# Kernel tuning notes

Hardware: AMD Instinct MI355X
Metric: run time of the kernel (lower is better)

The kernel has to match this reference:

```python
import jax, jax.numpy as jnp
import numpy as np

N, E, F_IN, H, L = 100000, 1600000, 256, 128, 4
ALPHA, THETA, EPS = 0.1, 0.5, 1e-5


def setup_inputs() -> dict:
    key = jax.random.key(0)
    ks = jax.random.split(key, 6)
    x = jax.random.normal(ks[0], (N, F_IN), dtype=jnp.float32)
    edge_index = jax.random.randint(ks[1], (2, E), 0, N, dtype=jnp.int32)
    lin0_w = jax.random.normal(ks[2], (F_IN, H), dtype=jnp.float32) / np.sqrt(F_IN)
    lin0_b = jnp.zeros((H,), dtype=jnp.float32)
    conv_w = jax.random.normal(ks[3], (L, H, H), dtype=jnp.float32) / np.sqrt(H)
    bn_gamma = jnp.ones((L - 1, H), dtype=jnp.float32)
    bn_beta = jnp.zeros((L - 1, H), dtype=jnp.float32)
    return {"x": x, "edge_index": edge_index, "lin0_w": lin0_w, "lin0_b": lin0_b,
            "conv_w": conv_w, "bn_gamma": bn_gamma, "bn_beta": bn_beta}


def reference(x, edge_index, lin0_w, lin0_b, conv_w, bn_gamma, bn_beta):
    n = x.shape[0]
    loops = jnp.arange(n, dtype=edge_index.dtype)
    row = jnp.concatenate([edge_index[0], loops])  # source
    col = jnp.concatenate([edge_index[1], loops])  # target
    # GCN symmetric normalization with self-loops: D^{-1/2}(A+I)D^{-1/2}
    deg = jax.ops.segment_sum(jnp.ones_like(col, dtype=x.dtype), col, num_segments=n)
    dinv = jnp.where(deg > 0, jax.lax.rsqrt(deg), 0.0)
    norm = (dinv[row] * dinv[col])[:, None]  # [E+N, 1]

    def prop(h):  # sparse aggregation: out[c] += norm * h[r]
        return jax.ops.segment_sum(h[row] * norm, col, num_segments=n)

    # GCNConv input layer
    z = prop(x @ lin0_w) + lin0_b
    x0 = z
    for i in range(L):
        h = prop(z)
        beta = float(np.log(THETA / (i + 1) + 1.0))
        s = (1.0 - ALPHA) * h + ALPHA * x0          # identity mapping to initial features
        z = (1.0 - beta) * s + beta * (s @ conv_w[i])  # shared_weights GCN2Conv
        if i < L - 1:
            mu = jnp.mean(z, axis=0)
            var = jnp.mean((z - mu) ** 2, axis=0)
            z = (z - mu) * jax.lax.rsqrt(var + EPS) * bn_gamma[i] + bn_beta[i]
            z = jax.nn.relu(z)
    return z
```

## Files before the change

kernel.cpp:

```cpp
#include <hip/hip_runtime.h>
#include <hip/hip_bf16.h>
#include <math.h>

#define H 128
#define EPS_BN 1e-5f
#define RSTATS 16

typedef __attribute__((ext_vector_type(8))) short short8;
typedef __attribute__((ext_vector_type(4))) float f32x4;

__device__ __forceinline__ float bf2f(ushort u){
  union { float f; uint v; } x; x.v = ((uint)u) << 16; return x.f;
}
__device__ __forceinline__ ushort f2bf(float f){
  union { float f; uint v; } x; x.f = f;
  uint v = x.v;
  uint r = v + 0x7fff + ((v >> 16) & 1);
  return (ushort)(r >> 16);
}

__device__ __forceinline__ void acc8(float* a, uint4 v, float wt){
  a[0] += wt*bf2f((ushort)(v.x & 0xffff)); a[1] += wt*bf2f((ushort)(v.x >> 16));
  a[2] += wt*bf2f((ushort)(v.y & 0xffff)); a[3] += wt*bf2f((ushort)(v.y >> 16));
  a[4] += wt*bf2f((ushort)(v.z & 0xffff)); a[5] += wt*bf2f((ushort)(v.z >> 16));
  a[6] += wt*bf2f((ushort)(v.w & 0xffff)); a[7] += wt*bf2f((ushort)(v.w >> 16));
}


__global__ void k_count(const int* __restrict__ col, int E, int* __restrict__ cnt){
  int i = blockIdx.x*blockDim.x + threadIdx.x;
  if (i < E) atomicAdd(&cnt[col[i]], 1);
}

__global__ void k_scan1(const int* __restrict__ cnt, int* __restrict__ off,
                        int* __restrict__ bsum, float* __restrict__ dinv, int n){
  __shared__ int s[1024];
  int t = threadIdx.x;
  int i = blockIdx.x*1024 + t;
  int v = (i < n) ? cnt[i] : 0;
  if (i < n) dinv[i] = rsqrtf((float)v + 1.0f);
  s[t] = v; __syncthreads();
  for (int d = 1; d < 1024; d <<= 1){
    int x = (t >= d) ? s[t-d] : 0;
    __syncthreads();
    s[t] += x;
    __syncthreads();
  }
  if (i < n) off[i] = s[t] - v;
  if (t == 1023) bsum[blockIdx.x] = s[1023];
}

__global__ void k_scan2(int* bsum, int nb){
  int l = threadIdx.x;
  int carry = 0;
  for (int b0 = 0; b0 < nb; b0 += 64){
    int i = b0 + l;
    int orig = (i < nb) ? bsum[i] : 0;
    int v = orig;
    #pragma unroll
    for (int d = 1; d < 64; d <<= 1){
      int x = __shfl_up(v, d);
      if (l >= d) v += x;
    }
    if (i < nb) bsum[i] = carry + v - orig;
    carry += __shfl(v, 63);
  }
}

__global__ void k_scan3(int* __restrict__ off, int* __restrict__ cursor,
                        const int* __restrict__ bsum, int n, int Etot){
  int i = blockIdx.x*blockDim.x + threadIdx.x;
  if (i < n){ int o = off[i] + bsum[i >> 10]; off[i] = o; cursor[i] = o; }
  if (i == 0) off[n] = Etot;
}

__global__ void k_fill(const int* __restrict__ row, const int* __restrict__ col, int E,
                       const float* __restrict__ dinv, int* __restrict__ cursor,
                       uint2* __restrict__ edge){
  int i = blockIdx.x*blockDim.x + threadIdx.x;
  if (i < E){
    int c = col[i], r = row[i];
    int p = atomicAdd(&cursor[c], 1);
    edge[p] = make_uint2((uint)r, __float_as_uint(dinv[r]*dinv[c]));
  }
}


__global__ __launch_bounds__(1024) void k_dhist(
    const int* __restrict__ cnt, int* __restrict__ dh, int n){
  __shared__ int lh[256];
  int t = threadIdx.x;
  if (t < 256) lh[t] = 0;
  __syncthreads();
  int i = blockIdx.x*1024 + t;
  if (i < n){
    int d = cnt[i]; if (d > 255) d = 255;
    atomicAdd(&lh[d], 1);
  }
  __syncthreads();
  if (t < 256 && lh[t]) atomicAdd(&dh[t], lh[t]);
}

__global__ void k_dscan(int* __restrict__ dh){
  __shared__ int s[256];
  int t = threadIdx.x;
  int v = dh[t];
  s[t] = v; __syncthreads();
  for (int d = 1; d < 256; d <<= 1){
    int x = (t >= d) ? s[t-d] : 0;
    __syncthreads();
    s[t] += x;
    __syncthreads();
  }
  dh[t] = s[t] - v;
}

__global__ __launch_bounds__(1024) void k_dperm(
    const int* __restrict__ cnt, int* __restrict__ dh,
    int* __restrict__ perm, int n){
  __shared__ int lh[256];
  __shared__ int lbase[256];
  int t = threadIdx.x;
  if (t < 256) lh[t] = 0;
  __syncthreads();
  int i = blockIdx.x*1024 + t;
  int d = 0, li = 0;
  if (i < n){
    d = cnt[i]; if (d > 255) d = 255;
    li = atomicAdd(&lh[d], 1);
  }
  __syncthreads();
  if (t < 256){
    int c = lh[t];
    lbase[t] = c ? atomicAdd(&dh[t], c) : 0;
  }
  __syncthreads();
  if (i < n) perm[lbase[d] + li] = i;
}


__global__ void k_prepw(const float* __restrict__ lin0_w, const float* __restrict__ conv_w,
                        ushort* __restrict__ lin0T, ushort* __restrict__ WpT,
                        float b0, float b1, float b2, float b3){
  int i = blockIdx.x*blockDim.x + threadIdx.x;
  if (i < 128*256){
    int nn = i >> 8, k = i & 255;
    lin0T[i] = f2bf(lin0_w[k*128 + nn]);
  } else if (i < 128*256 + 4*128*128){
    int j = i - 128*256;
    int ll = j >> 14, rc = j & 16383;
    int nn = rc >> 7, k = rc & 127;
    float beta = (ll==0)?b0:(ll==1)?b1:(ll==2)?b2:b3;
    float v = beta * conv_w[ll*16384 + k*128 + nn];
    if (k == nn) v += 1.0f - beta;
    WpT[j] = f2bf(v);
  }
}


__device__ __forceinline__ void gather_edges(
    float* a, const ushort* __restrict__ zin, const uint2* __restrict__ edge,
    int e0, int e1, int lr){
  int e = e0;
  for (; e + 3 < e1; e += 4){
    uint2 er0 = edge[e],   er1 = edge[e+1];
    uint2 er2 = edge[e+2], er3 = edge[e+3];
    uint4 v0 = *(const uint4*)(zin + (size_t)er0.x*H + lr*8);
    uint4 v1 = *(const uint4*)(zin + (size_t)er1.x*H + lr*8);
    uint4 v2 = *(const uint4*)(zin + (size_t)er2.x*H + lr*8);
    uint4 v3 = *(const uint4*)(zin + (size_t)er3.x*H + lr*8);
    acc8(a, v0, __uint_as_float(er0.y));
    acc8(a, v1, __uint_as_float(er1.y));
    acc8(a, v2, __uint_as_float(er2.y));
    acc8(a, v3, __uint_as_float(er3.y));
  }
  for (; e < e1; ++e){
    uint2 er = edge[e];
    uint4 v = *(const uint4*)(zin + (size_t)er.x*H + lr*8);
    acc8(a, v, __uint_as_float(er.y));
  }
}


__global__ __launch_bounds__(256) void k_prop0(
    const ushort* __restrict__ h, const int* __restrict__ off,
    const uint2* __restrict__ edge, const float* __restrict__ dinv,
    const float* __restrict__ bias, const int* __restrict__ perm,
    ushort* __restrict__ x0, int n){
  int pq = (blockIdx.x*blockDim.x + threadIdx.x) >> 4;
  if (pq >= n) return;
  int gq = perm[n - 1 - pq];
  int lr = threadIdx.x & 15;
  float a[8];
  #pragma unroll
  for (int j = 0; j < 8; ++j) a[j] = 0.f;
  float wc = dinv[gq]; wc *= wc;
  uint4 vs = *(const uint4*)(h + (size_t)gq*H + lr*8);
  gather_edges(a, h, edge, off[gq], off[gq+1], lr);
  acc8(a, vs, wc);
  float4 b0 = *(const float4*)(bias + lr*8);
  float4 b1 = *(const float4*)(bias + lr*8 + 4);
  uint4 pk;
  pk.x = (uint)f2bf(a[0]+b0.x) | ((uint)f2bf(a[1]+b0.y) << 16);
  pk.y = (uint)f2bf(a[2]+b0.z) | ((uint)f2bf(a[3]+b0.w) << 16);
  pk.z = (uint)f2bf(a[4]+b1.x) | ((uint)f2bf(a[5]+b1.y) << 16);
  pk.w = (uint)f2bf(a[6]+b1.z) | ((uint)f2bf(a[7]+b1.w) << 16);
  *(uint4*)(x0 + (size_t)gq*H + lr*8) = pk;
}


template<bool STATS, bool OUTF32, bool SAMEX0>
__global__ __launch_bounds__(256) void k_layer(
    const ushort* __restrict__ zin, const ushort* __restrict__ x0,
    const int* __restrict__ off, const uint2* __restrict__ edge,
    const float* __restrict__ dinv, const ushort* __restrict__ BT,
    const int* __restrict__ perm,
    void* __restrict__ zout, float* __restrict__ stats, int n)
{
  __shared__ ushort Sm[32*128];
  __shared__ int pm[32];
  int t = threadIdx.x;
  int w = t >> 6, l = t & 63;
  int lr = l & 15, q = l >> 4;
  int base = blockIdx.x * 32;
  if (t < 32) pm[t] = (base + t < n) ? perm[n - 1 - (base + t)] : -1;
  __syncthreads();

  #pragma unroll
  for (int g2 = 0; g2 < 2; ++g2){
    int row  = w*8 + g2*4 + q;
    int node = pm[row];
    float a[8];
    #pragma unroll
    for (int j = 0; j < 8; ++j) a[j] = 0.f;
    uint4 pk = make_uint4(0u,0u,0u,0u);
    if (node >= 0){
      float wc = dinv[node]; wc *= wc;
      uint4 vs = *(const uint4*)(zin + (size_t)node*H + lr*8);
      gather_edges(a, zin, edge, off[node], off[node+1], lr);
      acc8(a, vs, wc);
      uint4 xv = SAMEX0 ? vs : *(const uint4*)(x0 + (size_t)node*H + lr*8);
      float s0 = 0.9f*a[0] + 0.1f*bf2f((ushort)(xv.x & 0xffff));
      float s1 = 0.9f*a[1] + 0.1f*bf2f((ushort)(xv.x >> 16));
      float s2 = 0.9f*a[2] + 0.1f*bf2f((ushort)(xv.y & 0xffff));
      float s3 = 0.9f*a[3] + 0.1f*bf2f((ushort)(xv.y >> 16));
      float s4 = 0.9f*a[4] + 0.1f*bf2f((ushort)(xv.z & 0xffff));
      float s5 = 0.9f*a[5] + 0.1f*bf2f((ushort)(xv.z >> 16));
      float s6 = 0.9f*a[6] + 0.1f*bf2f((ushort)(xv.w & 0xffff));
      float s7 = 0.9f*a[7] + 0.1f*bf2f((ushort)(xv.w >> 16));
      pk.x = (uint)f2bf(s0) | ((uint)f2bf(s1) << 16);
      pk.y = (uint)f2bf(s2) | ((uint)f2bf(s3) << 16);
      pk.z = (uint)f2bf(s4) | ((uint)f2bf(s5) << 16);
      pk.w = (uint)f2bf(s6) | ((uint)f2bf(s7) << 16);
    }
    *(uint4*)(&Sm[row*128 + ((lr ^ (row & 15))*8)]) = pk;
  }

  short8 bfr[2][4];
  #pragma unroll
  for (int c = 0; c < 2; ++c)
    #pragma unroll
    for (int ks = 0; ks < 4; ++ks)
      bfr[c][ks] = *(const short8*)(BT + (size_t)(w*32 + c*16 + lr)*H + ks*32 + q*8);

  __syncthreads();

  f32x4 acc[2][2];
  #pragma unroll
  for (int rt = 0; rt < 2; ++rt){
    acc[rt][0] = (f32x4){0.f,0.f,0.f,0.f};
    acc[rt][1] = (f32x4){0.f,0.f,0.f,0.f};
  }
  #pragma unroll
  for (int rt = 0; rt < 2; ++rt){
    int row = rt*16 + lr;
    #pragma unroll
    for (int ks = 0; ks < 4; ++ks){
      short8 af = *(const short8*)(&Sm[row*128 + (((ks*4 + q) ^ (row & 15))*8)]);
      acc[rt][0] = __builtin_amdgcn_mfma_f32_16x16x32_bf16(af, bfr[0][ks], acc[rt][0], 0,0,0);
      acc[rt][1] = __builtin_amdgcn_mfma_f32_16x16x32_bf16(af, bfr[1][ks], acc[rt][1], 0,0,0);
    }
  }

  #pragma unroll
  for (int rt = 0; rt < 2; ++rt){
    #pragma unroll
    for (int c = 0; c < 2; ++c){
      #pragma unroll
      for (int j2 = 0; j2 < 4; ++j2){
        int rowl = rt*16 + q*4 + j2;
        int nodeo = pm[rowl];
        float v = acc[rt][c][j2];
        if (OUTF32){
          if (nodeo >= 0)
            ((float*)zout)[(size_t)nodeo*H + w*32 + c*16 + lr] = v;
        } else {
          float other = __shfl(v, l ^ 1);
          if (!(lr & 1) && nodeo >= 0){
            uint pk = (uint)f2bf(v) | ((uint)f2bf(other) << 16);
            ((uint*)zout)[(size_t)nodeo*64 + w*16 + c*8 + (lr >> 1)] = pk;
          }
        }
      }
    }
  }
  if (STATS){
    #pragma unroll
    for (int c = 0; c < 2; ++c){
      float sv = 0.f, sq = 0.f;
      #pragma unroll
      for (int rt = 0; rt < 2; ++rt)
        #pragma unroll
        for (int j2 = 0; j2 < 4; ++j2){
          float v = acc[rt][c][j2];
          sv += v; sq += v*v;
        }
      sv += __shfl(sv, l ^ 16); sv += __shfl(sv, l ^ 32);
      sq += __shfl(sq, l ^ 16); sq += __shfl(sq, l ^ 32);
      if (q == 0){
        float* st = stats + (size_t)(blockIdx.x & (RSTATS-1))*256;
        atomicAdd(&st[w*32 + c*16 + lr], sv);
        atomicAdd(&st[128 + w*32 + c*16 + lr], sq);
      }
    }
  }
}


__global__ void k_bnfinal(float* __restrict__ stats, const float* __restrict__ gamma,
                          const float* __restrict__ beta, float* __restrict__ scsh,
                          float inv_n){
  int f = threadIdx.x;
  float s = 0.f, s2 = 0.f;
  for (int r = 0; r < RSTATS; ++r){
    s  += stats[r*256 + f];
    s2 += stats[r*256 + 128 + f];
    stats[r*256 + f] = 0.f;
    stats[r*256 + 128 + f] = 0.f;
  }
  float mu  = s * inv_n;
  float var = s2 * inv_n - mu*mu;
  float sc  = rsqrtf(var + EPS_BN) * gamma[f];
  scsh[f]       = sc;
  scsh[128 + f] = beta[f] - mu*sc;
}


__global__ __launch_bounds__(256) void k_bnapply(
    uint4* __restrict__ z, const float* __restrict__ scsh, int n16){
  int i = blockIdx.x*blockDim.x + threadIdx.x;
  if (i >= n16) return;
  int f8 = (i & 15) * 8;
  uint4 v = z[i];
  uint r[4];
  #pragma unroll
  for (int p = 0; p < 4; ++p){
    uint  u  = (&v.x)[p];
    float z0 = bf2f((ushort)(u & 0xffff));
    float z1 = bf2f((ushort)(u >> 16));
    float y0 = fmaxf(fmaf(z0, scsh[f8 + p*2],     scsh[128 + f8 + p*2]),     0.f);
    float y1 = fmaxf(fmaf(z1, scsh[f8 + p*2 + 1], scsh[128 + f8 + p*2 + 1]), 0.f);
    r[p] = (uint)f2bf(y0) | ((uint)f2bf(y1) << 16);
  }
  z[i] = make_uint4(r[0], r[1], r[2], r[3]);
}


__global__ __launch_bounds__(256) void k_gemm0(
    const float* __restrict__ Af, const ushort* __restrict__ BT,
    ushort* __restrict__ Cb, int n){
  const int K = 256;
  __shared__ ushort As[64*32];
  __shared__ ushort Bs[128*32];
  int t = threadIdx.x;
  int br = blockIdx.x * 64;
  int w = t >> 6, l = t & 63;
  int lr = l & 15, lk = l >> 4;
  int swz = (lr >> 1) & 3;

  f32x4 acc[8];
  #pragma unroll
  for (int i = 0; i < 8; ++i) acc[i] = (f32x4){0.f,0.f,0.f,0.f};

  int sar = t >> 2;
  int sab = t & 3;
  int sa_off = sar*32 + ((sab ^ ((sar>>1)&3))*8);

  for (int k0 = 0; k0 < K; k0 += 32){
    int grow = br + sar;
    float4 v0 = make_float4(0.f,0.f,0.f,0.f), v1 = v0;
    if (grow < n){
      v0 = *(const float4*)(Af + (size_t)grow*K + k0 + sab*8);
      v1 = *(const float4*)(Af + (size_t)grow*K + k0 + sab*8 + 4);
    }
    ushort tmp[8] = {f2bf(v0.x),f2bf(v0.y),f2bf(v0.z),f2bf(v0.w),
                     f2bf(v1.x),f2bf(v1.y),f2bf(v1.z),f2bf(v1.w)};
    *(uint4*)(&As[sa_off]) = *(const uint4*)tmp;
    #pragma unroll
    for (int i = 0; i < 2; ++i){
      int qq = t + i*256;
      int nrow = qq >> 2, bb = qq & 3;
      uint4 v = *(const uint4*)(BT + (size_t)nrow*K + k0 + bb*8);
      *(uint4*)(&Bs[nrow*32 + ((bb ^ ((nrow>>1)&3))*8)]) = v;
    }
    __syncthreads();
    short8 af = *(const short8*)(&As[(w*16+lr)*32 + ((lk ^ swz)*8)]);
    #pragma unroll
    for (int tn = 0; tn < 8; ++tn){
      short8 bfv = *(const short8*)(&Bs[(tn*16+lr)*32 + ((lk ^ swz)*8)]);
      acc[tn] = __builtin_amdgcn_mfma_f32_16x16x32_bf16(af, bfv, acc[tn], 0, 0, 0);
    }
    __syncthreads();
  }
  int orow = br + w*16 + lk*4;
  #pragma unroll
  for (int tn = 0; tn < 8; ++tn){
    #pragma unroll
    for (int j = 0; j < 4; ++j){
      float mine  = acc[tn][j];
      float other = __shfl(mine, l ^ 1);
      if (!(l & 1) && (orow + j) < n){
        uint pk = (uint)f2bf(mine) | ((uint)f2bf(other) << 16);
        ((uint*)Cb)[(size_t)(orow+j)*64 + tn*8 + (lr >> 1)] = pk;
      }
    }
  }
}


extern "C" void kernel_launch(void* const* d_in, const int* in_sizes, int n_in,
                              void* d_out, int out_size, void* d_ws, size_t ws_size,
                              hipStream_t stream){
  const float* x        = (const float*)d_in[0];
  const int*   ei       = (const int*)  d_in[1];
  const float* lin0_w   = (const float*)d_in[2];
  const float* lin0_b   = (const float*)d_in[3];
  const float* conv_w   = (const float*)d_in[4];
  const float* bn_gamma = (const float*)d_in[5];
  const float* bn_beta  = (const float*)d_in[6];
  float* out = (float*)d_out;

  int N = in_sizes[0] / 256;
  int E = in_sizes[1] / 2;
  const int* row = ei;
  const int* col = ei + E;

  char* ws = (char*)d_ws;
  size_t p = 0;
  auto alloc = [&](size_t bytes)->char*{
    char* r = ws + p; p = (p + bytes + 255) & ~(size_t)255; return r;
  };
  int*    cnt    = (int*)   alloc((size_t)N*4);
  int*    off    = (int*)   alloc((size_t)(N+1)*4);
  int*    cursor = (int*)   alloc((size_t)N*4);
  float*  dinv   = (float*) alloc((size_t)N*4);
  int*    bsum   = (int*)   alloc(512*4);
  int*    dh     = (int*)   alloc(256*4);
  int*    perm   = (int*)   alloc((size_t)N*4);
  uint2*  edge   = (uint2*) alloc((size_t)E*8);
  ushort* zb     = (ushort*)alloc((size_t)N*H*2);
  ushort* sb     = (ushort*)alloc((size_t)N*H*2);
  ushort* x0b    = (ushort*)alloc((size_t)N*H*2);
  ushort* lin0T  = (ushort*)alloc(128*256*2);
  ushort* WpT    = (ushort*)alloc(4*128*128*2);
  float*  stats  = (float*) alloc(RSTATS*256*4);
  float*  scsh   = (float*) alloc(2*128*4);

  float betas[4];
  for (int i = 0; i < 4; ++i) betas[i] = logf(0.5f/(float)(i+1) + 1.0f);
  float inv_n = 1.0f/(float)N;

  hipMemsetAsync(cnt, 0, (size_t)N*4, stream);
  hipMemsetAsync(dh, 0, 256*4, stream);
  k_count<<<(E+255)/256, 256, 0, stream>>>(col, E, cnt);
  int nb1k = (N + 1023)/1024;
  k_dhist<<<nb1k, 1024, 0, stream>>>(cnt, dh, N);
  k_dscan<<<1, 256, 0, stream>>>(dh);
  k_dperm<<<nb1k, 1024, 0, stream>>>(cnt, dh, perm, N);
  k_scan1<<<nb1k, 1024, 0, stream>>>(cnt, off, bsum, dinv, N);
  k_scan2<<<1, 64, 0, stream>>>(bsum, nb1k);
  k_scan3<<<(N+255)/256, 256, 0, stream>>>(off, cursor, bsum, N, E);
  k_fill <<<(E+255)/256, 256, 0, stream>>>(row, col, E, dinv, cursor, edge);

  k_prepw<<<(128*256 + 4*128*128 + 255)/256, 256, 0, stream>>>(
      lin0_w, conv_w, lin0T, WpT, betas[0], betas[1], betas[2], betas[3]);

  int gemm_blocks = (N + 63)/64;
  int lay_blocks  = (N + 31)/32;
  int prop_blocks = (N + 15)/16;
  int bn_blocks   = ((N*16) + 255)/256;

  k_gemm0<<<gemm_blocks, 256, 0, stream>>>(x, lin0T, sb, N);
  k_prop0<<<prop_blocks, 256, 0, stream>>>(sb, off, edge, dinv, lin0_b, perm, x0b, N);

  hipMemsetAsync(stats, 0, RSTATS*256*4, stream);

  k_layer<true,false,true><<<lay_blocks, 256, 0, stream>>>(
      x0b, x0b, off, edge, dinv, WpT + 0*128*128, perm, sb, stats, N);
  k_bnfinal<<<1, 128, 0, stream>>>(stats, bn_gamma + 0*H, bn_beta + 0*H, scsh, inv_n);
  k_bnapply<<<bn_blocks, 256, 0, stream>>>((uint4*)sb, scsh, N*16);

  k_layer<true,false,false><<<lay_blocks, 256, 0, stream>>>(
      sb, x0b, off, edge, dinv, WpT + 1*128*128, perm, zb, stats, N);
  k_bnfinal<<<1, 128, 0, stream>>>(stats, bn_gamma + 1*H, bn_beta + 1*H, scsh, inv_n);
  k_bnapply<<<bn_blocks, 256, 0, stream>>>((uint4*)zb, scsh, N*16);

  k_layer<true,false,false><<<lay_blocks, 256, 0, stream>>>(
      zb, x0b, off, edge, dinv, WpT + 2*128*128, perm, sb, stats, N);
  k_bnfinal<<<1, 128, 0, stream>>>(stats, bn_gamma + 2*H, bn_beta + 2*H, scsh, inv_n);
  k_bnapply<<<bn_blocks, 256, 0, stream>>>((uint4*)sb, scsh, N*16);

  k_layer<false,true,false><<<lay_blocks, 256, 0, stream>>>(
      sb, x0b, off, edge, dinv, WpT + 3*128*128, perm, out, nullptr, N);
}
```

Baseline: 612.6 us.

## Store node features in degree-sorted permuted order to make self and output accesses contiguous

Intermediate feature buffers are now indexed by position in the degree-sorted permutation instead of the original node id. An inverse permutation is built so edge sources are stored as permuted indices. The degree scan is reversed so the perm array itself is descending and needs no n-1-i flip. The first GEMM gathers input rows through perm. Self-feature loads, x0 loads and bf16 output stores become contiguous per block, which removes scattered row accesses. Gather locality over neighbours changes with the new ordering, and the extra iperm array plus the perm lookup in the GEMM add a little setup cost.

New measurement: 603.2 us. Within noise of the previous version (-1.5%).

```diff
diff --git a/kernel.cpp b/kernel.cpp
--- a/kernel.cpp
+++ b/kernel.cpp
@@ -75,13 +75,13 @@
 }
 
 __global__ void k_fill(const int* __restrict__ row, const int* __restrict__ col, int E,
-                       const float* __restrict__ dinv, int* __restrict__ cursor,
-                       uint2* __restrict__ edge){
+                       const float* __restrict__ dinv, const int* __restrict__ iperm,
+                       int* __restrict__ cursor, uint2* __restrict__ edge){
   int i = blockIdx.x*blockDim.x + threadIdx.x;
   if (i < E){
     int c = col[i], r = row[i];
     int p = atomicAdd(&cursor[c], 1);
-    edge[p] = make_uint2((uint)r, __float_as_uint(dinv[r]*dinv[c]));
+    edge[p] = make_uint2((uint)iperm[r], __float_as_uint(dinv[r]*dinv[c]));
   }
 }
 
@@ -104,7 +104,7 @@
 __global__ void k_dscan(int* __restrict__ dh){
   __shared__ int s[256];
   int t = threadIdx.x;
-  int v = dh[t];
+  int v = dh[255 - t];
   s[t] = v; __syncthreads();
   for (int d = 1; d < 256; d <<= 1){
     int x = (t >= d) ? s[t-d] : 0;
@@ -112,12 +112,12 @@
     s[t] += x;
     __syncthreads();
   }
-  dh[t] = s[t] - v;
+  dh[255 - t] = s[t] - v;
 }
 
 __global__ __launch_bounds__(1024) void k_dperm(
     const int* __restrict__ cnt, int* __restrict__ dh,
-    int* __restrict__ perm, int n){
+    int* __restrict__ perm, int* __restrict__ iperm, int n){
   __shared__ int lh[256];
   __shared__ int lbase[256];
   int t = threadIdx.x;
@@ -135,7 +135,11 @@
     lbase[t] = c ? atomicAdd(&dh[t], c) : 0;
   }
   __syncthreads();
-  if (i < n) perm[lbase[d] + li] = i;
+  if (i < n){
+    int pos = lbase[d] + li;
+    perm[pos] = i;
+    iperm[i] = pos;
+  }
 }
 
 
@@ -189,13 +193,13 @@
     ushort* __restrict__ x0, int n){
   int pq = (blockIdx.x*blockDim.x + threadIdx.x) >> 4;
   if (pq >= n) return;
-  int gq = perm[n - 1 - pq];
+  int gq = perm[pq];
   int lr = threadIdx.x & 15;
   float a[8];
   #pragma unroll
   for (int j = 0; j < 8; ++j) a[j] = 0.f;
   float wc = dinv[gq]; wc *= wc;
-  uint4 vs = *(const uint4*)(h + (size_t)gq*H + lr*8);
+  uint4 vs = *(const uint4*)(h + (size_t)pq*H + lr*8);
   gather_edges(a, h, edge, off[gq], off[gq+1], lr);
   acc8(a, vs, wc);
   float4 b0 = *(const float4*)(bias + lr*8);
@@ -205,7 +209,7 @@
   pk.y = (uint)f2bf(a[2]+b0.z) | ((uint)f2bf(a[3]+b0.w) << 16);
   pk.z = (uint)f2bf(a[4]+b1.x) | ((uint)f2bf(a[5]+b1.y) << 16);
   pk.w = (uint)f2bf(a[6]+b1.z) | ((uint)f2bf(a[7]+b1.w) << 16);
-  *(uint4*)(x0 + (size_t)gq*H + lr*8) = pk;
+  *(uint4*)(x0 + (size_t)pq*H + lr*8) = pk;
 }
 
 
@@ -223,23 +227,24 @@
   int w = t >> 6, l = t & 63;
   int lr = l & 15, q = l >> 4;
   int base = blockIdx.x * 32;
-  if (t < 32) pm[t] = (base + t < n) ? perm[n - 1 - (base + t)] : -1;
+  if (t < 32) pm[t] = (base + t < n) ? perm[base + t] : -1;
   __syncthreads();
 
   #pragma unroll
   for (int g2 = 0; g2 < 2; ++g2){
     int row  = w*8 + g2*4 + q;
     int node = pm[row];
+    int grow = base + row;
     float a[8];
     #pragma unroll
     for (int j = 0; j < 8; ++j) a[j] = 0.f;
     uint4 pk = make_uint4(0u,0u,0u,0u);
     if (node >= 0){
       float wc = dinv[node]; wc *= wc;
-      uint4 vs = *(const uint4*)(zin + (size_t)node*H + lr*8);
+      uint4 vs = *(const uint4*)(zin + (size_t)grow*H + lr*8);
       gather_edges(a, zin, edge, off[node], off[node+1], lr);
       acc8(a, vs, wc);
-      uint4 xv = SAMEX0 ? vs : *(const uint4*)(x0 + (size_t)node*H + lr*8);
+      uint4 xv = SAMEX0 ? vs : *(const uint4*)(x0 + (size_t)grow*H + lr*8);
       float s0 = 0.9f*a[0] + 0.1f*bf2f((ushort)(xv.x & 0xffff));
       float s1 = 0.9f*a[1] + 0.1f*bf2f((ushort)(xv.x >> 16));
       float s2 = 0.9f*a[2] + 0.1f*bf2f((ushort)(xv.y & 0xffff));
@@ -289,16 +294,17 @@
       #pragma unroll
       for (int j2 = 0; j2 < 4; ++j2){
         int rowl = rt*16 + q*4 + j2;
-        int nodeo = pm[rowl];
         float v = acc[rt][c][j2];
         if (OUTF32){
+          int nodeo = pm[rowl];
           if (nodeo >= 0)
             ((float*)zout)[(size_t)nodeo*H + w*32 + c*16 + lr] = v;
         } else {
+          int growl = base + rowl;
           float other = __shfl(v, l ^ 1);
-          if (!(lr & 1) && nodeo >= 0){
+          if (!(lr & 1) && growl < n){
             uint pk = (uint)f2bf(v) | ((uint)f2bf(other) << 16);
-            ((uint*)zout)[(size_t)nodeo*64 + w*16 + c*8 + (lr >> 1)] = pk;
+            ((uint*)zout)[(size_t)growl*64 + w*16 + c*8 + (lr >> 1)] = pk;
           }
         }
       }
@@ -368,15 +374,18 @@
 
 __global__ __launch_bounds__(256) void k_gemm0(
     const float* __restrict__ Af, const ushort* __restrict__ BT,
-    ushort* __restrict__ Cb, int n){
+    const int* __restrict__ perm, ushort* __restrict__ Cb, int n){
   const int K = 256;
   __shared__ ushort As[64*32];
   __shared__ ushort Bs[128*32];
+  __shared__ int pmr[64];
   int t = threadIdx.x;
   int br = blockIdx.x * 64;
   int w = t >> 6, l = t & 63;
   int lr = l & 15, lk = l >> 4;
   int swz = (lr >> 1) & 3;
+  if (t < 64) pmr[t] = (br + t < n) ? perm[br + t] : -1;
+  __syncthreads();
 
   f32x4 acc[8];
   #pragma unroll
@@ -387,9 +396,9 @@
   int sa_off = sar*32 + ((sab ^ ((sar>>1)&3))*8);
 
   for (int k0 = 0; k0 < K; k0 += 32){
-    int grow = br + sar;
+    int grow = pmr[sar];
     float4 v0 = make_float4(0.f,0.f,0.f,0.f), v1 = v0;
-    if (grow < n){
+    if (grow >= 0){
       v0 = *(const float4*)(Af + (size_t)grow*K + k0 + sab*8);
       v1 = *(const float4*)(Af + (size_t)grow*K + k0 + sab*8 + 4);
     }
@@ -457,6 +466,7 @@
   int*    bsum   = (int*)   alloc(512*4);
   int*    dh     = (int*)   alloc(256*4);
   int*    perm   = (int*)   alloc((size_t)N*4);
+  int*    iperm  = (int*)   alloc((size_t)N*4);
   uint2*  edge   = (uint2*) alloc((size_t)E*8);
   ushort* zb     = (ushort*)alloc((size_t)N*H*2);
   ushort* sb     = (ushort*)alloc((size_t)N*H*2);
@@ -476,11 +486,11 @@
   int nb1k = (N + 1023)/1024;
   k_dhist<<<nb1k, 1024, 0, stream>>>(cnt, dh, N);
   k_dscan<<<1, 256, 0, stream>>>(dh);
-  k_dperm<<<nb1k, 1024, 0, stream>>>(cnt, dh, perm, N);
+  k_dperm<<<nb1k, 1024, 0, stream>>>(cnt, dh, perm, iperm, N);
   k_scan1<<<nb1k, 1024, 0, stream>>>(cnt, off, bsum, dinv, N);
   k_scan2<<<1, 64, 0, stream>>>(bsum, nb1k);
   k_scan3<<<(N+255)/256, 256, 0, stream>>>(off, cursor, bsum, N, E);
-  k_fill <<<(E+255)/256, 256, 0, stream>>>(row, col, E, dinv, cursor, edge);
+  k_fill <<<(E+255)/256, 256, 0, stream>>>(row, col, E, dinv, iperm, cursor, edge);
 
   k_prepw<<<(128*256 + 4*128*128 + 255)/256, 256, 0, stream>>>(
       lin0_w, conv_w, lin0T, WpT, betas[0], betas[1], betas[2], betas[3]);
@@ -490,7 +500,7 @@
   int prop_blocks = (N + 15)/16;
   int bn_blocks   = ((N*16) + 255)/256;
 
-  k_gemm0<<<gemm_blocks, 256, 0, stream>>>(x, lin0T, sb, N);
+  k_gemm0<<<gemm_blocks, 256, 0, stream>>>(x, lin0T, perm, sb, N);
   k_prop0<<<prop_blocks, 256, 0, stream>>>(sb, off, edge, dinv, lin0_b, perm, x0b, N);
 
   hipMemsetAsync(stats, 0, RSTATS*256*4, stream);
```
